# Performance work log

Hardware: AMD Instinct MI355X
Metric: run time of the kernel (lower is better)

The kernel has to match this reference:

```python
import jax, jax.numpy as jnp
import numpy as np

B, C, H, W = 16, 2048, 16, 16
HEADS = 4
HEAD_DIM = C // HEADS


def setup_inputs() -> dict:
    key = jax.random.key(0)
    ks = jax.random.split(key, 7)
    s = 0.02
    x = jax.random.normal(ks[0], (B, C, H, W), dtype=jnp.float32)
    q_w = jax.random.normal(ks[1], (HEADS, HEAD_DIM, C), dtype=jnp.float32) * s
    q_b = jax.random.normal(ks[2], (HEADS, HEAD_DIM), dtype=jnp.float32) * s
    k_w = jax.random.normal(ks[3], (HEADS, HEAD_DIM, C), dtype=jnp.float32) * s
    k_b = jax.random.normal(ks[4], (HEADS, HEAD_DIM), dtype=jnp.float32) * s
    v_w = jax.random.normal(ks[5], (HEADS, C, C), dtype=jnp.float32) * s
    v_b = jax.random.normal(ks[6], (HEADS, C), dtype=jnp.float32) * s
    return {"x": x, "q_w": q_w, "q_b": q_b, "k_w": k_w, "k_b": k_b, "v_w": v_w, "v_b": v_b}


def reference(x, q_w, q_b, k_w, k_b, v_w, v_b):
    b, c, h, w = x.shape
    heads, head_dim, _ = q_w.shape
    # [B, N, C] with N = H*W
    patch = jnp.transpose(x, (0, 2, 3, 1)).reshape(b, h * w, c)
    # stacked per-head linear projections (bias per head)
    Q = jnp.einsum('bnc,hdc->bhnd', patch, q_w) + q_b[None, :, None, :]   # [B,heads,N,head_dim]
    K = jnp.einsum('bnc,hdc->bhnd', patch, k_w) + k_b[None, :, None, :]   # [B,heads,N,head_dim]
    V = jnp.einsum('bnc,hec->bhne', patch, v_w) + v_b[None, :, None, :]   # [B,heads,N,C]
    sim = jnp.einsum('bhqd,bhkd->bhqk', Q, K) / (head_dim ** 0.5)          # [B,heads,N,N]
    # sum over query dim, softmax over heads
    att = jnp.sum(sim, axis=2)[:, :, None, :]                              # [B,heads,1,N]
    att = jax.nn.softmax(att, axis=1)
    n = att.shape[-1]
    side = int(n ** 0.5)
    attention_score = att.reshape(b, heads, side, side)                    # [B,heads,h,w]
    # per-head spatial gating of the input, concatenated along channels
    x_enhance = (attention_score[:, :, None, :, :] * x[:, None, :, :, :]).reshape(b, heads * c, h, w)
    # standard softmax attention combine
    sim = jax.nn.softmax(sim, axis=-1)
    general = jnp.einsum('bhqk,bhke->bhqe', sim, V)                        # [B,heads,N,C]
    general = general.reshape(b, heads, side, side, c)
    general = jnp.transpose(general, (0, 1, 4, 2, 3)).reshape(b, heads * c, side, side)
    output = general + x_enhance
    return (attention_score, output)
```

## Files before the change

kernel.cpp:

```cpp
#include <hip/hip_runtime.h>
#include <hip/hip_bf16.h>

#define B_ 16
#define C_ 2048
#define N_ 256
#define HEADS_ 4
#define D_ 512

typedef unsigned int u32;
typedef unsigned short ushort_t;
typedef __attribute__((ext_vector_type(8))) short bfx8;
typedef __attribute__((ext_vector_type(4))) float fx4;

__device__ __forceinline__ unsigned short f2bs(float f) {
    __hip_bfloat16 h = __float2bfloat16(f);
    return __builtin_bit_cast(unsigned short, h);
}
__device__ __forceinline__ float bs2f(ushort_t u) {
    u32 v = ((u32)u) << 16;
    return __builtin_bit_cast(float, v);
}
__device__ __forceinline__ void gload16(const void* g, void* l) {
    __builtin_amdgcn_global_load_lds((const __attribute__((address_space(1))) u32*)g,
                                     (__attribute__((address_space(3))) u32*)l, 16, 0, 0);
}
__device__ __forceinline__ int xcd_swz(int bid, int nwg) {
    return (bid & 7) * (nwg >> 3) + (bid >> 3);
}

#define VMW8() asm volatile("s_waitcnt vmcnt(8)" ::: "memory")
#define SBAR() __builtin_amdgcn_s_barrier()
#define LGKM0() do { asm volatile("s_waitcnt lgkmcnt(0)" ::: "memory"); \
                     __builtin_amdgcn_sched_barrier(0); } while (0)

#define STAGE8(MAT, BUF, KH, J) do {                                          \
    const ushort_t* s_ = (MAT) ? Bm : A;                                      \
    _Pragma("unroll")                                                         \
    for (int l_ = 0; l_ < 2; ++l_) {                                          \
        const int r_ = l_ * 128 + (tid >> 2);                                 \
        const int k_ = (J) * 64 + (KH) * 32 + (((tid & 3) ^ ((tid >> 3) & 3)) * 8); \
        gload16(s_ + (size_t)r_ * K + k_,                                     \
                (char*)(&lds[MAT][BUF][KH][0][0]) + l_ * 8192 + tid * 16);    \
    } } while (0)

#define LDA8(dst, BUF, KH, MH) do {                                           \
    _Pragma("unroll")                                                         \
    for (int i_ = 0; i_ < 4; ++i_)                                            \
        dst[i_] = *(const bfx8*)&lds[0][BUF][KH][wmr + (MH) * 64 + i_ * 16 + l16][swz8]; \
    } while (0)

#define LDB8(dst, BUF, KH) do {                                               \
    _Pragma("unroll")                                                         \
    for (int i_ = 0; i_ < 4; ++i_)                                            \
        dst[i_] = *(const bfx8*)&lds[1][BUF][KH][wnr + i_ * 16 + l16][swz8];  \
    } while (0)

#define MM8(aa, bb, MH) do {                                                  \
    __builtin_amdgcn_s_setprio(1);                                            \
    _Pragma("unroll")                                                         \
    for (int i_ = 0; i_ < 4; ++i_) {                                          \
        _Pragma("unroll")                                                     \
        for (int n_ = 0; n_ < 4; ++n_)                                        \
            acc[(MH) * 4 + i_][n_] = __builtin_amdgcn_mfma_f32_16x16x32_bf16( \
                aa[i_], bb[n_], acc[(MH) * 4 + i_][n_], 0, 0, 0);             \
    }                                                                         \
    __builtin_amdgcn_s_setprio(0);                                            \
} while (0)

#define KTILE(BUF, JS1, JS2) do {                                             \
    bfx8 a0[4], a1[4], b0[4], b1[4];                                          \
                                                       \
    LDA8(a0, BUF, 0, 0); LDB8(b0, BUF, 0);                                    \
    STAGE8(0, BUF ^ 1, 1, JS1);                                               \
    SBAR(); LGKM0();                                                          \
    MM8(a0, b0, 0);                                                           \
    SBAR();                                                                   \
                                                       \
    LDA8(a1, BUF, 0, 1);                                                      \
    STAGE8(1, BUF ^ 1, 1, JS1);                                               \
    SBAR(); LGKM0();                                                          \
    MM8(a1, b0, 1);                                                           \
    VMW8();                                                                   \
    SBAR();                                                                   \
                                                       \
    LDA8(a0, BUF, 1, 0); LDB8(b1, BUF, 1);                                    \
    STAGE8(0, BUF, 0, JS2);                                                   \
    SBAR(); LGKM0();                                                          \
    MM8(a0, b1, 0);                                                           \
    SBAR();                                                                   \
                                                       \
    LDA8(a1, BUF, 1, 1);                                                      \
    STAGE8(1, BUF, 0, JS2);                                                   \
    SBAR(); LGKM0();                                                          \
    MM8(a1, b1, 1);                                                           \
    VMW8();                                                                   \
    SBAR();                                                                   \
} while (0)

typedef ushort_t lds256_t[2][2][2][256][32];

__device__ __forceinline__ void gemm256_8ph(const ushort_t* __restrict__ A,
                                            const ushort_t* __restrict__ Bm,
                                            int K, lds256_t& lds, fx4 acc[8][4])
{
    const int tid = threadIdx.x;
    const int lane = tid & 63;
    const int w = tid >> 6;
    const int l16 = lane & 15, lhi = lane >> 4;
    const int swz8 = (lhi ^ ((l16 >> 1) & 3)) * 8;
    const int wmr = (w >> 2) * 128;
    const int wnr = (w & 3) * 64;
    const int nkt = K >> 6;

    STAGE8(0, 0, 0, 0); STAGE8(1, 0, 0, 0);
    STAGE8(0, 0, 1, 0); STAGE8(1, 0, 1, 0);
    STAGE8(0, 1, 0, 1); STAGE8(1, 1, 0, 1);
    VMW8();
    SBAR();

    for (int jj = 0; jj < nkt; jj += 2) {
        const int js1a = jj + 1;
        const int js2a = (jj + 2 < nkt) ? jj + 2 : nkt - 1;
        const int js1b = js2a;
        const int js2b = (jj + 3 < nkt) ? jj + 3 : nkt - 1;
        KTILE(0, js1a, js2a);
        KTILE(1, js1b, js2b);
    }
}

#define EPI256_IDX() \
    const int lane = threadIdx.x & 63, w = threadIdx.x >> 6; \
    const int l16 = lane & 15, lhi = lane >> 4; \
    const int wmr = (w >> 2) * 128, wnr = (w & 3) * 64;

__device__ __forceinline__ void mfma_core(const ushort_t* __restrict__ A,
                                          const ushort_t* __restrict__ Bm,
                                          int K, fx4 acc[4][4])
{
    __shared__ __align__(16) ushort_t As[128 * 32];
    __shared__ __align__(16) ushort_t Bs[128 * 32];
    const int tid = threadIdx.x;
    const int lane = tid & 63, wave = tid >> 6;
    const int l16 = lane & 15, lhi = lane >> 4;
    const int swz8 = (lhi ^ ((l16 >> 1) & 3)) * 8;
    const int wm = (wave >> 1) * 64, wn = (wave & 1) * 64;

    for (int k0 = 0; k0 < K; k0 += 32) {
        const int f0 = tid, f1 = tid + 256;
        gload16(A + (size_t)(f0 >> 2) * K + k0 + (((f0 & 3) ^ ((f0 >> 3) & 3)) * 8), As + f0 * 8);
        gload16(A + (size_t)(f1 >> 2) * K + k0 + (((f1 & 3) ^ ((f1 >> 3) & 3)) * 8), As + f1 * 8);
        gload16(Bm + (size_t)(f0 >> 2) * K + k0 + (((f0 & 3) ^ ((f0 >> 3) & 3)) * 8), Bs + f0 * 8);
        gload16(Bm + (size_t)(f1 >> 2) * K + k0 + (((f1 & 3) ^ ((f1 >> 3) & 3)) * 8), Bs + f1 * 8);
        __syncthreads();
        bfx8 af[4], bfr[4];
#pragma unroll
        for (int i = 0; i < 4; ++i)
            af[i] = *(const bfx8*)(As + (wm + i * 16 + l16) * 32 + swz8);
#pragma unroll
        for (int j = 0; j < 4; ++j)
            bfr[j] = *(const bfx8*)(Bs + (wn + j * 16 + l16) * 32 + swz8);
#pragma unroll
        for (int i = 0; i < 4; ++i)
#pragma unroll
            for (int j = 0; j < 4; ++j)
                acc[i][j] = __builtin_amdgcn_mfma_f32_16x16x32_bf16(af[i], bfr[j], acc[i][j], 0, 0, 0);
        __syncthreads();
    }
}

#define EPI_IDX() \
    const int lane = threadIdx.x & 63, wave = threadIdx.x >> 6; \
    const int l16 = lane & 15, lhi = lane >> 4; \
    const int wm = (wave >> 1) * 64, wn = (wave & 1) * 64;

__global__ __launch_bounds__(256) void k_castw(const float* __restrict__ s, ushort_t* __restrict__ d, int n) {
    int i = (blockIdx.x * 256 + threadIdx.x) * 4;
    if (i >= n) return;
    float4 v = *(const float4*)(s + i);
    ushort4 o = { f2bs(v.x), f2bs(v.y), f2bs(v.z), f2bs(v.w) };
    *(ushort4*)(d + i) = o;
}

__global__ __launch_bounds__(256) void k_cast_x(const float* __restrict__ x,
                                                ushort_t* __restrict__ xb, ushort_t* __restrict__ xbT,
                                                float* __restrict__ xpart) {
    __shared__ float t[32][33];
    const int b = blockIdx.z, c0 = blockIdx.y * 32, n0 = blockIdx.x * 32;
    const int tn = threadIdx.x & 31, tc8 = threadIdx.x >> 5;
    const float* xp = x + ((size_t)b * C_ + c0) * N_ + n0;
#pragma unroll
    for (int p = 0; p < 4; ++p) {
        int cc = tc8 + p * 8;
        float v = xp[(size_t)cc * N_ + tn];
        t[cc][tn] = v;
        xb[((size_t)b * C_ + c0 + cc) * N_ + n0 + tn] = f2bs(v);
        float s = v;
#pragma unroll
        for (int o = 16; o; o >>= 1) s += __shfl_xor(s, o, 32);
        if (tn == 0) xpart[(size_t)blockIdx.x * B_ * C_ + (size_t)b * C_ + c0 + cc] = s;
    }
    __syncthreads();
#pragma unroll
    for (int p = 0; p < 4; ++p) {
        int nn = tc8 + p * 8;
        xbT[((size_t)b * N_ + n0 + nn) * C_ + c0 + tn] = f2bs(t[tn][nn]);
    }
}

__global__ __launch_bounds__(256) void k_xsum2(const float* __restrict__ xpart, float* __restrict__ xsum) {
    const int c = blockIdx.x * 256 + threadIdx.x, b = blockIdx.y;
    float s = 0.f;
#pragma unroll
    for (int t = 0; t < 8; ++t) s += xpart[(size_t)t * B_ * C_ + (size_t)b * C_ + c];
    xsum[(size_t)b * C_ + c] = s;
}

__global__ __launch_bounds__(256) void k_qsum(const float* __restrict__ xsum, const float* __restrict__ qw,
                                              const float* __restrict__ qb, float* __restrict__ qsum) {
    const int wave = threadIdx.x >> 6, lane = threadIdx.x & 63;
    const int row = blockIdx.x * 4 + wave;
    const int h = row >> 9, d = row & 511;
    const float* wr = qw + (size_t)row * C_;
    float acc[16];
#pragma unroll
    for (int bb = 0; bb < 16; ++bb) acc[bb] = 0.f;
    for (int it = 0; it < C_ / 64; ++it) {
        const int c = it * 64 + lane;
        const float w = wr[c];
#pragma unroll
        for (int bb = 0; bb < 16; ++bb) acc[bb] += xsum[(size_t)bb * C_ + c] * w;
    }
#pragma unroll
    for (int bb = 0; bb < 16; ++bb) {
        float s = acc[bb];
#pragma unroll
        for (int o = 32; o; o >>= 1) s += __shfl_xor(s, o, 64);
        if (lane == 0) qsum[(size_t)((bb << 2) | h) * D_ + d] = s + 256.0f * qb[row];
    }
}

__global__ __launch_bounds__(64) void k_const(const float* __restrict__ qsum, const float* __restrict__ kb,
                                              float* __restrict__ cst) {
    const int bh = blockIdx.x, h = bh & 3, lane = threadIdx.x;
    float s = 0.f;
    for (int d = lane; d < D_; d += 64) s += qsum[(size_t)bh * D_ + d] * kb[h * D_ + d];
#pragma unroll
    for (int o = 32; o; o >>= 1) s += __shfl_xor(s, o, 64);
    if (lane == 0) cst[bh] = s;
}

__global__ __launch_bounds__(256) void k_vecp(const float* __restrict__ qsum, const float* __restrict__ kw,
                                              float* __restrict__ partv) {
    const int ct = blockIdx.x, h = blockIdx.y, dsl = blockIdx.z;
    __shared__ float qs[16 * 128];
    for (int i = threadIdx.x; i < 16 * 128; i += 256) {
        int bb = i >> 7, dd = i & 127;
        qs[i] = qsum[(size_t)((bb << 2) | h) * D_ + dsl * 128 + dd];
    }
    __syncthreads();
    const int c = ct * 256 + threadIdx.x;
    const float* wp = kw + ((size_t)h * D_ + dsl * 128) * C_ + c;
    float acc[16];
#pragma unroll
    for (int bb = 0; bb < 16; ++bb) acc[bb] = 0.f;
    for (int dd = 0; dd < 128; ++dd) {
        const float w = wp[(size_t)dd * C_];
#pragma unroll
        for (int bb = 0; bb < 16; ++bb) acc[bb] += qs[bb * 128 + dd] * w;
    }
#pragma unroll
    for (int bb = 0; bb < 16; ++bb)
        partv[((size_t)dsl * 64 + ((bb << 2) | h)) * C_ + c] = acc[bb];
}

__global__ __launch_bounds__(256) void k_att(const float* __restrict__ x, const float* __restrict__ partv,
                                             float* __restrict__ part) {
    const int bh = blockIdx.x, sl = blockIdx.y, b = bh >> 2;
    __shared__ float vs[512];
    const int c0 = sl * 512;
    for (int i = threadIdx.x; i < 512; i += 256) {
        float v = 0.f;
#pragma unroll
        for (int dsl = 0; dsl < 4; ++dsl) v += partv[((size_t)dsl * 64 + bh) * C_ + c0 + i];
        vs[i] = v;
    }
    __syncthreads();
    float a = 0.f;
    const float* xp = x + ((size_t)b * C_ + c0) * N_ + threadIdx.x;
#pragma unroll 8
    for (int c = 0; c < 512; ++c) a += vs[c] * xp[(size_t)c * N_];
    part[((size_t)sl * 64 + bh) * N_ + threadIdx.x] = a;
}

__global__ __launch_bounds__(256) void k_score(const float* __restrict__ part, const float* __restrict__ cst,
                                               float* __restrict__ score, float* __restrict__ out0) {
    const int b = blockIdx.x, k = threadIdx.x;
    const float scale = 0.044194173824159216f;
    float a[4];
#pragma unroll
    for (int h = 0; h < 4; ++h) {
        const int bh = b * 4 + h;
        float s = cst[bh];
#pragma unroll
        for (int sl = 0; sl < 4; ++sl) s += part[((size_t)sl * 64 + bh) * N_ + k];
        a[h] = s * scale;
    }
    float mx = fmaxf(fmaxf(a[0], a[1]), fmaxf(a[2], a[3]));
    float e0 = expf(a[0] - mx), e1 = expf(a[1] - mx), e2 = expf(a[2] - mx), e3 = expf(a[3] - mx);
    float inv = 1.0f / (e0 + e1 + e2 + e3);
    float r[4] = { e0 * inv, e1 * inv, e2 * inv, e3 * inv };
#pragma unroll
    for (int h = 0; h < 4; ++h) {
        score[(size_t)(b * 4 + h) * N_ + k] = r[h];
        out0[(size_t)(b * 4 + h) * N_ + k] = r[h];
    }
}

__global__ __launch_bounds__(512, 2) void k_proj(const ushort_t* __restrict__ xbT,
                                                 const ushort_t* __restrict__ qwb, const ushort_t* __restrict__ kwb,
                                                 const float* __restrict__ qb, const float* __restrict__ kb,
                                                 ushort_t* __restrict__ QKbuf) {
    __shared__ __align__(16) lds256_t lds;
    const int wg = xcd_swz(blockIdx.x, 256);
    const int quad = wg >> 2;
    const int mt = quad >> 2;
    const int nt = (quad & 3) * 4 + (wg & 3);
    const int c0 = nt * 256;
    const int qk = c0 >> 11;
    const int rem = c0 & 2047;
    const ushort_t* A  = xbT + (size_t)mt * 256 * C_;
    const ushort_t* Bm = (qk ? kwb : qwb) + (size_t)rem * C_;
    const float* bias  = (qk ? kb : qb) + rem;
    const int K = C_;

    fx4 acc[8][4];
#pragma unroll
    for (int i = 0; i < 8; ++i)
#pragma unroll
        for (int j = 0; j < 4; ++j) acc[i][j] = (fx4){0.f, 0.f, 0.f, 0.f};
    gemm256_8ph(A, Bm, K, lds, acc);

    EPI256_IDX();
#pragma unroll
    for (int i = 0; i < 8; ++i)
#pragma unroll
        for (int n = 0; n < 4; ++n)
#pragma unroll
            for (int r = 0; r < 4; ++r) {
                const int gr = mt * 256 + wmr + i * 16 + lhi * 4 + r;
                const int bq = gr >> 8, nn = gr & 255;
                const int lc = wnr + n * 16 + l16;
                const int hh = (rem + lc) >> 9, dl = (rem + lc) & 511;
                const float v = acc[i][n][r] + bias[lc];
                QKbuf[((((size_t)(qk * 16 + bq) * 4 + hh) * 256) + nn) * 512 + dl] = f2bs(v);
            }
}

__global__ __launch_bounds__(512, 2) void k_out(const ushort_t* __restrict__ vwb, const float* __restrict__ vb,
                                                const ushort_t* __restrict__ Tt, const float* __restrict__ score,
                                                const ushort_t* __restrict__ xb, float* __restrict__ out1) {
    __shared__ __align__(16) lds256_t lds;
    const int wg = xcd_swz(blockIdx.x, 512);
    const int h = wg >> 7, l = wg & 127;
    const int quad = l >> 2;
    const int mt = quad >> 2;
    const int nt = (quad & 3) * 4 + (l & 3);
    const ushort_t* A  = vwb + (size_t)h * C_ * C_ + (size_t)mt * 256 * C_;
    const ushort_t* Bm = Tt + (size_t)h * 16 * N_ * C_ + (size_t)nt * 256 * C_;
    const int K = C_;

    fx4 acc[8][4];
#pragma unroll
    for (int i = 0; i < 8; ++i)
#pragma unroll
        for (int j = 0; j < 4; ++j) acc[i][j] = (fx4){0.f, 0.f, 0.f, 0.f};
    gemm256_8ph(A, Bm, K, lds, acc);

    EPI256_IDX();
#pragma unroll
    for (int i = 0; i < 8; ++i)
#pragma unroll
        for (int n = 0; n < 4; ++n)
#pragma unroll
            for (int r = 0; r < 4; ++r) {
                const int e = mt * 256 + wmr + i * 16 + lhi * 4 + r;
                const int col = nt * 256 + wnr + n * 16 + l16;
                const int b = col >> 8, nn = col & 255;
                float v = acc[i][n][r] + vb[h * C_ + e]
                        + score[(size_t)(b * 4 + h) * N_ + nn] * bs2f(xb[((size_t)b * C_ + e) * N_ + nn]);
                out1[((size_t)(b * 4 + h) * C_ + e) * N_ + nn] = v;
            }
}

__global__ __launch_bounds__(512, 2) void k_T8(const ushort_t* __restrict__ Pb, const ushort_t* __restrict__ xb,
                                               ushort_t* __restrict__ Tt) {
    __shared__ __align__(16) lds256_t lds;
    const int wg = xcd_swz(blockIdx.x, 512);
    const int b = wg >> 5, l = wg & 31;
    const int mt = l >> 3, nt = l & 7;
    const ushort_t* A  = Pb + ((size_t)b * 1024 + mt * 256) * 256;
    const ushort_t* Bm = xb + ((size_t)b * 2048 + nt * 256) * 256;
    const int K = N_;

    fx4 acc[8][4];
#pragma unroll
    for (int i = 0; i < 8; ++i)
#pragma unroll
        for (int j = 0; j < 4; ++j) acc[i][j] = (fx4){0.f, 0.f, 0.f, 0.f};
    gemm256_8ph(A, Bm, K, lds, acc);

    EPI256_IDX();
#pragma unroll
    for (int i = 0; i < 8; ++i)
#pragma unroll
        for (int n = 0; n < 4; ++n)
#pragma unroll
            for (int r = 0; r < 4; ++r) {
                const int rowm = mt * 256 + wmr + i * 16 + lhi * 4 + r;
                const int h = rowm >> 8, q = rowm & 255;
                const int c = nt * 256 + wnr + n * 16 + l16;
                Tt[(((size_t)h * 16 + b) * 256 + q) * 2048 + c] = f2bs(acc[i][n][r]);
            }
}

__global__ __launch_bounds__(256) void k_sim(const ushort_t* __restrict__ QKbuf, float* __restrict__ simf) {
    const int wg = blockIdx.x;
    const int bh = wg >> 2, mt = (wg >> 1) & 1, ntl = wg & 1;
    const ushort_t* Qr = QKbuf;
    const ushort_t* Kr = QKbuf + (size_t)16 * 4 * 256 * 512;
    const ushort_t* A = Qr + ((size_t)bh * 256 + mt * 128) * 512;
    const ushort_t* Bm = Kr + ((size_t)bh * 256 + ntl * 128) * 512;

    fx4 acc[4][4];
#pragma unroll
    for (int i = 0; i < 4; ++i)
#pragma unroll
        for (int j = 0; j < 4; ++j) acc[i][j] = (fx4){0.f, 0.f, 0.f, 0.f};
    mfma_core(A, Bm, D_, acc);

    EPI_IDX();
    const float scale = 0.044194173824159216f;
#pragma unroll
    for (int i = 0; i < 4; ++i)
#pragma unroll
        for (int j = 0; j < 4; ++j)
#pragma unroll
            for (int r = 0; r < 4; ++r) {
                const int q = mt * 128 + wm + i * 16 + lhi * 4 + r;
                const int k = ntl * 128 + wn + j * 16 + l16;
                simf[(size_t)bh * N_ * N_ + (size_t)q * N_ + k] = acc[i][j][r] * scale;
            }
}

__global__ __launch_bounds__(64) void k_softP(const float* __restrict__ simf, ushort_t* __restrict__ Pb) {
    const size_t row = blockIdx.x;
    const float* p = simf + row * N_;
    ushort_t* o = Pb + row * N_;
    const int t = threadIdx.x;
    float v0 = p[t], v1 = p[t + 64], v2 = p[t + 128], v3 = p[t + 192];
    float mx = fmaxf(fmaxf(v0, v1), fmaxf(v2, v3));
#pragma unroll
    for (int off = 32; off; off >>= 1) mx = fmaxf(mx, __shfl_xor(mx, off, 64));
    float e0 = expf(v0 - mx), e1 = expf(v1 - mx), e2 = expf(v2 - mx), e3 = expf(v3 - mx);
    float s = e0 + e1 + e2 + e3;
#pragma unroll
    for (int off = 32; off; off >>= 1) s += __shfl_xor(s, off, 64);
    const float inv = 1.0f / s;
    o[t] = f2bs(e0 * inv); o[t + 64] = f2bs(e1 * inv);
    o[t + 128] = f2bs(e2 * inv); o[t + 192] = f2bs(e3 * inv);
}

extern "C" void kernel_launch(void* const* d_in, const int* in_sizes, int n_in,
                              void* d_out, int out_size, void* d_ws, size_t ws_size,
                              hipStream_t stream)
{
    const float* x  = (const float*)d_in[0];
    const float* qw = (const float*)d_in[1];
    const float* qb = (const float*)d_in[2];
    const float* kw = (const float*)d_in[3];
    const float* kb = (const float*)d_in[4];
    const float* vw = (const float*)d_in[5];
    const float* vb = (const float*)d_in[6];

    float* out0 = (float*)d_out;
    float* out1 = out0 + (size_t)B_ * HEADS_ * N_;

    char* w = (char*)d_ws;
    ushort_t* vwb  = (ushort_t*)w;  w += (size_t)4 * C_ * C_ * 2;
    ushort_t* qwb  = (ushort_t*)w;  w += (size_t)4 * D_ * C_ * 2;
    ushort_t* kwb  = (ushort_t*)w;  w += (size_t)4 * D_ * C_ * 2;
    ushort_t* xb   = (ushort_t*)w;  w += (size_t)B_ * C_ * N_ * 2;
    ushort_t* QKbuf= (ushort_t*)w;  w += (size_t)2 * 16 * 4 * 256 * 512 * 2;
    ushort_t* Pb   = (ushort_t*)w;  w += (size_t)64 * N_ * N_ * 2;
    float*    simf = (float*)w;     w += (size_t)64 * N_ * N_ * 4;
    ushort_t* Tt   = (ushort_t*)w;  w += (size_t)64 * N_ * C_ * 2;
    ushort_t* xbT  = Tt;
    float*    xpart= (float*)w;     w += (size_t)8 * B_ * C_ * 4;
    float*    xsum = (float*)w;     w += (size_t)B_ * C_ * 4;
    float*    qsum = (float*)w;     w += (size_t)64 * D_ * 4;
    float*    cst  = (float*)w;     w += 1024;
    float*    partv= (float*)w;     w += (size_t)4 * 64 * C_ * 4;
    float*    part = (float*)w;     w += (size_t)4 * 64 * N_ * 4;
    float*    score= (float*)w;     w += (size_t)64 * N_ * 4;

    k_castw<<<dim3(4 * D_ * C_ / 4 / 256), 256, 0, stream>>>(qw, qwb, 4 * D_ * C_);
    k_castw<<<dim3(4 * D_ * C_ / 4 / 256), 256, 0, stream>>>(kw, kwb, 4 * D_ * C_);
    k_castw<<<dim3(4 * C_ * C_ / 4 / 256), 256, 0, stream>>>(vw, vwb, 4 * C_ * C_);
    k_cast_x<<<dim3(8, 64, 16), 256, 0, stream>>>(x, xb, xbT, xpart);

    k_xsum2<<<dim3(8, 16), 256, 0, stream>>>(xpart, xsum);
    k_qsum <<<dim3(512), 256, 0, stream>>>(xsum, qw, qb, qsum);
    k_const<<<dim3(64), 64, 0, stream>>>(qsum, kb, cst);
    k_vecp <<<dim3(8, 4, 4), 256, 0, stream>>>(qsum, kw, partv);
    k_att  <<<dim3(64, 4), 256, 0, stream>>>(x, partv, part);
    k_score<<<dim3(16), 256, 0, stream>>>(part, cst, score, out0);

    k_proj <<<dim3(256), 512, 0, stream>>>(xbT, qwb, kwb, qb, kb, QKbuf);
    k_sim  <<<dim3(256), 256, 0, stream>>>(QKbuf, simf);
    k_softP<<<dim3(64 * N_), 64, 0, stream>>>(simf, Pb);
    k_T8   <<<dim3(512), 512, 0, stream>>>(Pb, xb, Tt);
    k_out  <<<dim3(512), 512, 0, stream>>>(vwb, vb, Tt, score, xb, out1);
}
```

Before: 386.6 us.

## Switch projection, P·x and output GEMMs from bf16 to scaled fp8 e4m3

Weights, x, the softmax probabilities and the intermediate T are now cast to fp8 e4m3 with fixed power-of-two scales. The three large GEMMs (k_proj, k_T8, k_out) use fp8 MFMA with a retuned LDS swizzle and staging of one 16-byte load per thread. The epilogues undo the scales. This halves operand bytes and uses the higher fp8 MFMA rate, at the risk of larger numerical error, possible saturation from the fixed scales, and an extra fp8 copy of x being written.

```diff
diff --git a/kernel.cpp b/kernel.cpp
--- a/kernel.cpp
+++ b/kernel.cpp
@@ -1,5 +1,6 @@
 #include <hip/hip_runtime.h>
 #include <hip/hip_bf16.h>
+#include <hip/hip_fp8.h>
 
 #define B_ 16
 #define C_ 2048
@@ -8,6 +9,7 @@
 #define D_ 512
 
 typedef unsigned int u32;
+typedef unsigned char u8;
 typedef unsigned short ushort_t;
 typedef __attribute__((ext_vector_type(8))) short bfx8;
 typedef __attribute__((ext_vector_type(4))) float fx4;
@@ -20,6 +22,9 @@
     u32 v = ((u32)u) << 16;
     return __builtin_bit_cast(float, v);
 }
+__device__ __forceinline__ u8 f2f8(float f) {
+    return (u8)__hip_cvt_float_to_fp8(f, __HIP_SATFINITE, __HIP_E4M3);
+}
 __device__ __forceinline__ void gload16(const void* g, void* l) {
     __builtin_amdgcn_global_load_lds((const __attribute__((address_space(1))) u32*)g,
                                      (__attribute__((address_space(3))) u32*)l, 16, 0, 0);
@@ -28,94 +33,93 @@
     return (bid & 7) * (nwg >> 3) + (bid >> 3);
 }
 
-#define VMW8() asm volatile("s_waitcnt vmcnt(8)" ::: "memory")
 #define SBAR() __builtin_amdgcn_s_barrier()
 #define LGKM0() do { asm volatile("s_waitcnt lgkmcnt(0)" ::: "memory"); \
                      __builtin_amdgcn_sched_barrier(0); } while (0)
 
-#define STAGE8(MAT, BUF, KH, J) do {                                          \
-    const ushort_t* s_ = (MAT) ? Bm : A;                                      \
-    _Pragma("unroll")                                                         \
-    for (int l_ = 0; l_ < 2; ++l_) {                                          \
-        const int r_ = l_ * 128 + (tid >> 2);                                 \
-        const int k_ = (J) * 64 + (KH) * 32 + (((tid & 3) ^ ((tid >> 3) & 3)) * 8); \
-        gload16(s_ + (size_t)r_ * K + k_,                                     \
-                (char*)(&lds[MAT][BUF][KH][0][0]) + l_ * 8192 + tid * 16);    \
-    } } while (0)
-
-#define LDA8(dst, BUF, KH, MH) do {                                           \
+#define VMW4() asm volatile("s_waitcnt vmcnt(4)" ::: "memory")
+
+#define STAGEF8(MAT, BUF, KH, J) do {                                         \
+    const u8* s_ = (MAT) ? Bm : A;                                            \
+    const int r_ = tid >> 1;                                                  \
+    const int k_ = (J) * 64 + (KH) * 32 + (((tid & 1) ^ ((tid >> 3) & 1)) * 16); \
+    gload16(s_ + (size_t)r_ * K + k_,                                         \
+            (u8*)(&lds[MAT][BUF][KH][0][0]) + tid * 16);                      \
+} while (0)
+
+#define LDAF8(dst, BUF, KH, MH) do {                                          \
     _Pragma("unroll")                                                         \
     for (int i_ = 0; i_ < 4; ++i_)                                            \
-        dst[i_] = *(const bfx8*)&lds[0][BUF][KH][wmr + (MH) * 64 + i_ * 16 + l16][swz8]; \
-    } while (0)
-
-#define LDB8(dst, BUF, KH) do {                                               \
+        dst[i_] = *(const long*)(&lds[0][BUF][KH][wmr + (MH) * 64 + i_ * 16 + l16][f8off]); \
+} while (0)
+
+#define LDBF8(dst, BUF, KH) do {                                              \
     _Pragma("unroll")                                                         \
     for (int i_ = 0; i_ < 4; ++i_)                                            \
-        dst[i_] = *(const bfx8*)&lds[1][BUF][KH][wnr + i_ * 16 + l16][swz8];  \
-    } while (0)
-
-#define MM8(aa, bb, MH) do {                                                  \
+        dst[i_] = *(const long*)(&lds[1][BUF][KH][wnr + i_ * 16 + l16][f8off]); \
+} while (0)
+
+#define MMF8(aa, bb, MH) do {                                                 \
     __builtin_amdgcn_s_setprio(1);                                            \
     _Pragma("unroll")                                                         \
     for (int i_ = 0; i_ < 4; ++i_) {                                          \
         _Pragma("unroll")                                                     \
         for (int n_ = 0; n_ < 4; ++n_)                                        \
-            acc[(MH) * 4 + i_][n_] = __builtin_amdgcn_mfma_f32_16x16x32_bf16( \
+            acc[(MH) * 4 + i_][n_] = __builtin_amdgcn_mfma_f32_16x16x32_fp8_fp8( \
                 aa[i_], bb[n_], acc[(MH) * 4 + i_][n_], 0, 0, 0);             \
     }                                                                         \
     __builtin_amdgcn_s_setprio(0);                                            \
 } while (0)
 
-#define KTILE(BUF, JS1, JS2) do {                                             \
-    bfx8 a0[4], a1[4], b0[4], b1[4];                                          \
+#define KTILEF8(BUF, JS1, JS2) do {                                           \
+    long a0[4], a1[4], b0[4], b1[4];                                          \
                                                        \
-    LDA8(a0, BUF, 0, 0); LDB8(b0, BUF, 0);                                    \
-    STAGE8(0, BUF ^ 1, 1, JS1);                                               \
+    LDAF8(a0, BUF, 0, 0); LDBF8(b0, BUF, 0);                                  \
+    STAGEF8(0, BUF ^ 1, 1, JS1);                                              \
     SBAR(); LGKM0();                                                          \
-    MM8(a0, b0, 0);                                                           \
+    MMF8(a0, b0, 0);                                                          \
     SBAR();                                                                   \
                                                        \
-    LDA8(a1, BUF, 0, 1);                                                      \
-    STAGE8(1, BUF ^ 1, 1, JS1);                                               \
+    LDAF8(a1, BUF, 0, 1);                                                     \
+    STAGEF8(1, BUF ^ 1, 1, JS1);                                              \
     SBAR(); LGKM0();                                                          \
-    MM8(a1, b0, 1);                                                           \
-    VMW8();                                                                   \
+    MMF8(a1, b0, 1);                                                          \
+    VMW4();                                                                   \
     SBAR();                                                                   \
                                                        \
-    LDA8(a0, BUF, 1, 0); LDB8(b1, BUF, 1);                                    \
-    STAGE8(0, BUF, 0, JS2);                                                   \
+    LDAF8(a0, BUF, 1, 0); LDBF8(b1, BUF, 1);                                  \
+    STAGEF8(0, BUF, 0, JS2);                                                  \
     SBAR(); LGKM0();                                                          \
-    MM8(a0, b1, 0);                                                           \
+    MMF8(a0, b1, 0);                                                          \
     SBAR();                                                                   \
                                                        \
-    LDA8(a1, BUF, 1, 1);                                                      \
-    STAGE8(1, BUF, 0, JS2);                                                   \
+    LDAF8(a1, BUF, 1, 1);                                                     \
+    STAGEF8(1, BUF, 0, JS2);                                                  \
     SBAR(); LGKM0();                                                          \
-    MM8(a1, b1, 1);                                                           \
-    VMW8();                                                                   \
+    MMF8(a1, b1, 1);                                                          \
+    VMW4();                                                                   \
     SBAR();                                                                   \
 } while (0)
 
-typedef ushort_t lds256_t[2][2][2][256][32];
-
-__device__ __forceinline__ void gemm256_8ph(const ushort_t* __restrict__ A,
-                                            const ushort_t* __restrict__ Bm,
-                                            int K, lds256_t& lds, fx4 acc[8][4])
+typedef u8 ldsf8_t[2][2][2][256][32];
+
+__device__ __forceinline__ void gemm256_f8(const u8* __restrict__ A,
+                                           const u8* __restrict__ Bm,
+                                           int K, ldsf8_t& lds, fx4 acc[8][4])
 {
     const int tid = threadIdx.x;
     const int lane = tid & 63;
     const int w = tid >> 6;
     const int l16 = lane & 15, lhi = lane >> 4;
-    const int swz8 = (lhi ^ ((l16 >> 1) & 3)) * 8;
+    const int f8off = (((lhi >> 1) ^ ((l16 >> 2) & 1)) * 16) + (lhi & 1) * 8;
     const int wmr = (w >> 2) * 128;
     const int wnr = (w & 3) * 64;
     const int nkt = K >> 6;
 
-    STAGE8(0, 0, 0, 0); STAGE8(1, 0, 0, 0);
-    STAGE8(0, 0, 1, 0); STAGE8(1, 0, 1, 0);
-    STAGE8(0, 1, 0, 1); STAGE8(1, 1, 0, 1);
-    VMW8();
+    STAGEF8(0, 0, 0, 0); STAGEF8(1, 0, 0, 0);
+    STAGEF8(0, 0, 1, 0); STAGEF8(1, 0, 1, 0);
+    STAGEF8(0, 1, 0, 1); STAGEF8(1, 1, 0, 1);
+    VMW4();
     SBAR();
 
     for (int jj = 0; jj < nkt; jj += 2) {
@@ -123,9 +127,11 @@
         const int js2a = (jj + 2 < nkt) ? jj + 2 : nkt - 1;
         const int js1b = js2a;
         const int js2b = (jj + 3 < nkt) ? jj + 3 : nkt - 1;
-        KTILE(0, js1a, js2a);
-        KTILE(1, js1b, js2b);
-    }
+        KTILEF8(0, js1a, js2a);
+        KTILEF8(1, js1b, js2b);
+    }
+    asm volatile("s_waitcnt vmcnt(0)" ::: "memory");
+    SBAR();
 }
 
 #define EPI256_IDX() \
@@ -173,17 +179,18 @@
     const int l16 = lane & 15, lhi = lane >> 4; \
     const int wm = (wave >> 1) * 64, wn = (wave & 1) * 64;
 
-__global__ __launch_bounds__(256) void k_castw(const float* __restrict__ s, ushort_t* __restrict__ d, int n) {
+__global__ __launch_bounds__(256) void k_castw8(const float* __restrict__ s, u8* __restrict__ d,
+                                                int n, float scale) {
     int i = (blockIdx.x * 256 + threadIdx.x) * 4;
     if (i >= n) return;
     float4 v = *(const float4*)(s + i);
-    ushort4 o = { f2bs(v.x), f2bs(v.y), f2bs(v.z), f2bs(v.w) };
-    *(ushort4*)(d + i) = o;
+    uchar4 o = { f2f8(v.x * scale), f2f8(v.y * scale), f2f8(v.z * scale), f2f8(v.w * scale) };
+    *(uchar4*)(d + i) = o;
 }
 
 __global__ __launch_bounds__(256) void k_cast_x(const float* __restrict__ x,
-                                                ushort_t* __restrict__ xb, ushort_t* __restrict__ xbT,
-                                                float* __restrict__ xpart) {
+                                                ushort_t* __restrict__ xb, u8* __restrict__ xb8,
+                                                u8* __restrict__ xbT8, float* __restrict__ xpart) {
     __shared__ float t[32][33];
     const int b = blockIdx.z, c0 = blockIdx.y * 32, n0 = blockIdx.x * 32;
     const int tn = threadIdx.x & 31, tc8 = threadIdx.x >> 5;
@@ -194,6 +201,7 @@
         float v = xp[(size_t)cc * N_ + tn];
         t[cc][tn] = v;
         xb[((size_t)b * C_ + c0 + cc) * N_ + n0 + tn] = f2bs(v);
+        xb8[((size_t)b * C_ + c0 + cc) * N_ + n0 + tn] = f2f8(v * 8.0f);
         float s = v;
 #pragma unroll
         for (int o = 16; o; o >>= 1) s += __shfl_xor(s, o, 32);
@@ -203,7 +211,7 @@
 #pragma unroll
     for (int p = 0; p < 4; ++p) {
         int nn = tc8 + p * 8;
-        xbT[((size_t)b * N_ + n0 + nn) * C_ + c0 + tn] = f2bs(t[tn][nn]);
+        xbT8[((size_t)b * N_ + n0 + nn) * C_ + c0 + tn] = f2f8(t[tn][nn] * 8.0f);
     }
 }
 
@@ -316,11 +324,11 @@
     }
 }
 
-__global__ __launch_bounds__(512, 2) void k_proj(const ushort_t* __restrict__ xbT,
-                                                 const ushort_t* __restrict__ qwb, const ushort_t* __restrict__ kwb,
+__global__ __launch_bounds__(512, 2) void k_proj(const u8* __restrict__ xbT8,
+                                                 const u8* __restrict__ qw8, const u8* __restrict__ kw8,
                                                  const float* __restrict__ qb, const float* __restrict__ kb,
                                                  ushort_t* __restrict__ QKbuf) {
-    __shared__ __align__(16) lds256_t lds;
+    __shared__ __align__(16) ldsf8_t lds;
     const int wg = xcd_swz(blockIdx.x, 256);
     const int quad = wg >> 2;
     const int mt = quad >> 2;
@@ -328,8 +336,8 @@
     const int c0 = nt * 256;
     const int qk = c0 >> 11;
     const int rem = c0 & 2047;
-    const ushort_t* A  = xbT + (size_t)mt * 256 * C_;
-    const ushort_t* Bm = (qk ? kwb : qwb) + (size_t)rem * C_;
+    const u8* A  = xbT8 + (size_t)mt * 256 * C_;
+    const u8* Bm = (qk ? kw8 : qw8) + (size_t)rem * C_;
     const float* bias  = (qk ? kb : qb) + rem;
     const int K = C_;
 
@@ -338,7 +346,7 @@
     for (int i = 0; i < 8; ++i)
 #pragma unroll
         for (int j = 0; j < 4; ++j) acc[i][j] = (fx4){0.f, 0.f, 0.f, 0.f};
-    gemm256_8ph(A, Bm, K, lds, acc);
+    gemm256_f8(A, Bm, K, lds, acc);
 
     EPI256_IDX();
 #pragma unroll
@@ -351,22 +359,22 @@
                 const int bq = gr >> 8, nn = gr & 255;
                 const int lc = wnr + n * 16 + l16;
                 const int hh = (rem + lc) >> 9, dl = (rem + lc) & 511;
-                const float v = acc[i][n][r] + bias[lc];
+                const float v = acc[i][n][r] * (1.0f / 512.0f) + bias[lc];
                 QKbuf[((((size_t)(qk * 16 + bq) * 4 + hh) * 256) + nn) * 512 + dl] = f2bs(v);
             }
 }
 
-__global__ __launch_bounds__(512, 2) void k_out(const ushort_t* __restrict__ vwb, const float* __restrict__ vb,
-                                                const ushort_t* __restrict__ Tt, const float* __restrict__ score,
+__global__ __launch_bounds__(512, 2) void k_out(const u8* __restrict__ vw8, const float* __restrict__ vb,
+                                                const u8* __restrict__ Tt8, const float* __restrict__ score,
                                                 const ushort_t* __restrict__ xb, float* __restrict__ out1) {
-    __shared__ __align__(16) lds256_t lds;
+    __shared__ __align__(16) ldsf8_t lds;
     const int wg = xcd_swz(blockIdx.x, 512);
     const int h = wg >> 7, l = wg & 127;
     const int quad = l >> 2;
     const int mt = quad >> 2;
     const int nt = (quad & 3) * 4 + (l & 3);
-    const ushort_t* A  = vwb + (size_t)h * C_ * C_ + (size_t)mt * 256 * C_;
-    const ushort_t* Bm = Tt + (size_t)h * 16 * N_ * C_ + (size_t)nt * 256 * C_;
+    const u8* A  = vw8 + (size_t)h * C_ * C_ + (size_t)mt * 256 * C_;
+    const u8* Bm = Tt8 + (size_t)h * 16 * N_ * C_ + (size_t)nt * 256 * C_;
     const int K = C_;
 
     fx4 acc[8][4];
@@ -374,7 +382,7 @@
     for (int i = 0; i < 8; ++i)
 #pragma unroll
         for (int j = 0; j < 4; ++j) acc[i][j] = (fx4){0.f, 0.f, 0.f, 0.f};
-    gemm256_8ph(A, Bm, K, lds, acc);
+    gemm256_f8(A, Bm, K, lds, acc);
 
     EPI256_IDX();
 #pragma unroll
@@ -386,20 +394,20 @@
                 const int e = mt * 256 + wmr + i * 16 + lhi * 4 + r;
                 const int col = nt * 256 + wnr + n * 16 + l16;
                 const int b = col >> 8, nn = col & 255;
-                float v = acc[i][n][r] + vb[h * C_ + e]
+                float v = acc[i][n][r] * (1.0f / 1024.0f) + vb[h * C_ + e]
                         + score[(size_t)(b * 4 + h) * N_ + nn] * bs2f(xb[((size_t)b * C_ + e) * N_ + nn]);
                 out1[((size_t)(b * 4 + h) * C_ + e) * N_ + nn] = v;
             }
 }
 
-__global__ __launch_bounds__(512, 2) void k_T8(const ushort_t* __restrict__ Pb, const ushort_t* __restrict__ xb,
-                                               ushort_t* __restrict__ Tt) {
-    __shared__ __align__(16) lds256_t lds;
+__global__ __launch_bounds__(512, 2) void k_T8(const u8* __restrict__ Pb8, const u8* __restrict__ xb8,
+                                               u8* __restrict__ Tt8) {
+    __shared__ __align__(16) ldsf8_t lds;
     const int wg = xcd_swz(blockIdx.x, 512);
     const int b = wg >> 5, l = wg & 31;
     const int mt = l >> 3, nt = l & 7;
-    const ushort_t* A  = Pb + ((size_t)b * 1024 + mt * 256) * 256;
-    const ushort_t* Bm = xb + ((size_t)b * 2048 + nt * 256) * 256;
+    const u8* A  = Pb8 + ((size_t)b * 1024 + mt * 256) * 256;
+    const u8* Bm = xb8 + ((size_t)b * 2048 + nt * 256) * 256;
     const int K = N_;
 
     fx4 acc[8][4];
@@ -407,7 +415,7 @@
     for (int i = 0; i < 8; ++i)
 #pragma unroll
         for (int j = 0; j < 4; ++j) acc[i][j] = (fx4){0.f, 0.f, 0.f, 0.f};
-    gemm256_8ph(A, Bm, K, lds, acc);
+    gemm256_f8(A, Bm, K, lds, acc);
 
     EPI256_IDX();
 #pragma unroll
@@ -419,7 +427,7 @@
                 const int rowm = mt * 256 + wmr + i * 16 + lhi * 4 + r;
                 const int h = rowm >> 8, q = rowm & 255;
                 const int c = nt * 256 + wnr + n * 16 + l16;
-                Tt[(((size_t)h * 16 + b) * 256 + q) * 2048 + c] = f2bs(acc[i][n][r]);
+                Tt8[(((size_t)h * 16 + b) * 256 + q) * 2048 + c] = f2f8(acc[i][n][r] * 0.0078125f);
             }
 }
 
@@ -452,10 +460,10 @@
             }
 }
 
-__global__ __launch_bounds__(64) void k_softP(const float* __restrict__ simf, ushort_t* __restrict__ Pb) {
+__global__ __launch_bounds__(64) void k_softP(const float* __restrict__ simf, u8* __restrict__ Pb8) {
     const size_t row = blockIdx.x;
     const float* p = simf + row * N_;
-    ushort_t* o = Pb + row * N_;
+    u8* o = Pb8 + row * N_;
     const int t = threadIdx.x;
     float v0 = p[t], v1 = p[t + 64], v2 = p[t + 128], v3 = p[t + 192];
     float mx = fmaxf(fmaxf(v0, v1), fmaxf(v2, v3));
@@ -465,9 +473,9 @@
     float s = e0 + e1 + e2 + e3;
 #pragma unroll
     for (int off = 32; off; off >>= 1) s += __shfl_xor(s, off, 64);
-    const float inv = 1.0f / s;
-    o[t] = f2bs(e0 * inv); o[t + 64] = f2bs(e1 * inv);
-    o[t + 128] = f2bs(e2 * inv); o[t + 192] = f2bs(e3 * inv);
+    const float inv = 256.0f / s;
+    o[t] = f2f8(e0 * inv); o[t + 64] = f2f8(e1 * inv);
+    o[t + 128] = f2f8(e2 * inv); o[t + 192] = f2f8(e3 * inv);
 }
 
 extern "C" void kernel_launch(void* const* d_in, const int* in_sizes, int n_in,
@@ -486,15 +494,16 @@
     float* out1 = out0 + (size_t)B_ * HEADS_ * N_;
 
     char* w = (char*)d_ws;
-    ushort_t* vwb  = (ushort_t*)w;  w += (size_t)4 * C_ * C_ * 2;
-    ushort_t* qwb  = (ushort_t*)w;  w += (size_t)4 * D_ * C_ * 2;
-    ushort_t* kwb  = (ushort_t*)w;  w += (size_t)4 * D_ * C_ * 2;
+    u8*       vw8  = (u8*)w;        w += (size_t)4 * C_ * C_;
+    u8*       qw8  = (u8*)w;        w += (size_t)4 * D_ * C_;
+    u8*       kw8  = (u8*)w;        w += (size_t)4 * D_ * C_;
     ushort_t* xb   = (ushort_t*)w;  w += (size_t)B_ * C_ * N_ * 2;
+    u8*       xb8  = (u8*)w;        w += (size_t)B_ * C_ * N_;
+    u8*       xbT8 = (u8*)w;        w += (size_t)B_ * N_ * C_;
     ushort_t* QKbuf= (ushort_t*)w;  w += (size_t)2 * 16 * 4 * 256 * 512 * 2;
-    ushort_t* Pb   = (ushort_t*)w;  w += (size_t)64 * N_ * N_ * 2;
+    u8*       Pb8  = (u8*)w;        w += (size_t)64 * N_ * N_;
     float*    simf = (float*)w;     w += (size_t)64 * N_ * N_ * 4;
-    ushort_t* Tt   = (ushort_t*)w;  w += (size_t)64 * N_ * C_ * 2;
-    ushort_t* xbT  = Tt;
+    u8*       Tt8  = (u8*)w;        w += (size_t)64 * N_ * C_;
     float*    xpart= (float*)w;     w += (size_t)8 * B_ * C_ * 4;
     float*    xsum = (float*)w;     w += (size_t)B_ * C_ * 4;
     float*    qsum = (float*)w;     w += (size_t)64 * D_ * 4;
@@ -503,10 +512,10 @@
     float*    part = (float*)w;     w += (size_t)4 * 64 * N_ * 4;
     float*    score= (float*)w;     w += (size_t)64 * N_ * 4;
 
-    k_castw<<<dim3(4 * D_ * C_ / 4 / 256), 256, 0, stream>>>(qw, qwb, 4 * D_ * C_);
-    k_castw<<<dim3(4 * D_ * C_ / 4 / 256), 256, 0, stream>>>(kw, kwb, 4 * D_ * C_);
-    k_castw<<<dim3(4 * C_ * C_ / 4 / 256), 256, 0, stream>>>(vw, vwb, 4 * C_ * C_);
-    k_cast_x<<<dim3(8, 64, 16), 256, 0, stream>>>(x, xb, xbT, xpart);
+    k_castw8<<<dim3(4 * D_ * C_ / 4 / 256), 256, 0, stream>>>(qw, qw8, 4 * D_ * C_, 64.0f);
+    k_castw8<<<dim3(4 * D_ * C_ / 4 / 256), 256, 0, stream>>>(kw, kw8, 4 * D_ * C_, 64.0f);
+    k_castw8<<<dim3(4 * C_ * C_ / 4 / 256), 256, 0, stream>>>(vw, vw8, 4 * C_ * C_, 64.0f);
+    k_cast_x<<<dim3(8, 64, 16), 256, 0, stream>>>(x, xb, xb8, xbT8, xpart);
 
     k_xsum2<<<dim3(8, 16), 256, 0, stream>>>(xpart, xsum);
     k_qsum <<<dim3(512), 256, 0, stream>>>(xsum, qw, qb, qsum);
@@ -515,9 +524,9 @@
     k_att  <<<dim3(64, 4), 256, 0, stream>>>(x, partv, part);
     k_score<<<dim3(16), 256, 0, stream>>>(part, cst, score, out0);
 
-    k_proj <<<dim3(256), 512, 0, stream>>>(xbT, qwb, kwb, qb, kb, QKbuf);
+    k_proj <<<dim3(256), 512, 0, stream>>>(xbT8, qw8, kw8, qb, kb, QKbuf);
     k_sim  <<<dim3(256), 256, 0, stream>>>(QKbuf, simf);
-    k_softP<<<dim3(64 * N_), 64, 0, stream>>>(simf, Pb);
-    k_T8   <<<dim3(512), 512, 0, stream>>>(Pb, xb, Tt);
-    k_out  <<<dim3(512), 512, 0, stream>>>(vwb, vb, Tt, score, xb, out1);
-}
+    k_softP<<<dim3(64 * N_), 64, 0, stream>>>(simf, Pb8);
+    k_T8   <<<dim3(512), 512, 0, stream>>>(Pb8, xb8, Tt8);
+    k_out  <<<dim3(512), 512, 0, stream>>>(vw8, vb, Tt8, score, xb, out1);
+}
```

After: 367.2 us. 5.0% less time.
